# Optimization experiments

Hardware: AMD Instinct MI355X
Metric: run time of the kernel (lower is better)

## Reference

```python
import jax, jax.numpy as jnp
import numpy as np

N0, N1, B = 260000, 10240, 1024
E0, E1 = 256000, 10240
IN_C, HID, OUT_C = 602, 256, 41


def setup_inputs() -> dict:
    key = jax.random.key(0)
    ks = jax.random.split(key, 12)
    x = jax.random.normal(ks[0], (N0, IN_C), dtype=jnp.float32)
    W_l0 = jax.random.normal(ks[1], (IN_C, HID), dtype=jnp.float32) / np.sqrt(IN_C)
    b_l0 = jnp.zeros((HID,), dtype=jnp.float32)
    W_r0 = jax.random.normal(ks[2], (IN_C, HID), dtype=jnp.float32) / np.sqrt(IN_C)
    W_l1 = jax.random.normal(ks[3], (HID, OUT_C), dtype=jnp.float32) / np.sqrt(HID)
    b_l1 = jnp.zeros((OUT_C,), dtype=jnp.float32)
    W_r1 = jax.random.normal(ks[4], (HID, OUT_C), dtype=jnp.float32) / np.sqrt(HID)
    src0 = jax.random.randint(ks[5], (E0,), 0, N0)
    dst0 = jnp.sort(jax.random.randint(ks[6], (E0,), 0, N1))
    src1 = jax.random.randint(ks[7], (E1,), 0, N1)
    dst1 = jnp.sort(jax.random.randint(ks[8], (E1,), 0, B))
    return {"x": x, "W_l0": W_l0, "b_l0": b_l0, "W_r0": W_r0,
            "W_l1": W_l1, "b_l1": b_l1, "W_r1": W_r1,
            "src0": src0, "dst0": dst0, "src1": src1, "dst1": dst1}


def _sage_conv(x_src, x_tgt, src, dst, num_tgt, W_l, b_l, W_r):
    # mean aggregation of neighbor messages (PyG SAGEConv, mean aggr)
    msg = x_src[src]                                             # [E, C]
    s = jax.ops.segment_sum(msg, dst, num_segments=num_tgt)     # [Nt, C]
    cnt = jax.ops.segment_sum(jnp.ones((src.shape[0], 1), x_src.dtype),
                              dst, num_segments=num_tgt)         # [Nt, 1]
    agg = s / jnp.maximum(cnt, 1.0)
    # out = lin_l(agg) + lin_r(x_target); lin_r has no bias in PyG
    return agg @ W_l + b_l + x_tgt @ W_r


def reference(x, W_l0, b_l0, W_r0, W_l1, b_l1, W_r1, src0, dst0, src1, dst1):
    # layer 0: N0 sources -> N1 targets (targets are first N1 rows of x)
    h = _sage_conv(x, x[:N1], src0, dst0, N1, W_l0, b_l0, W_r0)
    h = jax.nn.relu(h)  # dropout is identity in eval mode
    # layer 1: N1 sources -> B targets
    out = _sage_conv(h, h[:B], src1, dst1, B, W_l1, b_l1, W_r1)
    return jax.nn.log_softmax(out, axis=-1)
```

## Files before the change

kernel.cpp:

```cpp
#include <hip/hip_runtime.h>
#include <hip/hip_bf16.h>
#include <math.h>

constexpr int cN1  = 10240;
constexpr int cB   = 1024;
constexpr int cE0  = 256000;
constexpr int cE1  = 10240;
constexpr int cIN  = 602;
constexpr int cHID = 256;
constexpr int cOUT = 41;
constexpr int KC   = 1216;

typedef __attribute__((ext_vector_type(8))) short short8;
typedef __attribute__((ext_vector_type(4))) float f32x4;

__device__ __forceinline__ int lower_bound_dev(const int* __restrict__ a, int n, int v) {
    int l = 0, r = n;
    while (l < r) { int m = (l + r) >> 1; if (a[m] < v) l = m + 1; else r = m; }
    return l;
}

__global__ __launch_bounds__(256) void k_agg0(
    const float* __restrict__ x, const int* __restrict__ src0,
    const int* __restrict__ dst0, __hip_bfloat16* __restrict__ cat)
{
    const int t   = blockIdx.x;
    const int tid = threadIdx.x;
    const int lo  = lower_bound_dev(dst0, cE0, t);
    const int hi  = lower_bound_dev(dst0, cE0, t + 1);
    const int cnt = hi - lo;

    float a0 = 0.f, a1 = 0.f, a2 = 0.f;
    __shared__ int s_src[256];
    for (int base = lo; base < hi; base += 256) {
        const int n = min(256, hi - base);
        __syncthreads();
        if (tid < n) s_src[tid] = src0[base + tid];
        __syncthreads();
        for (int j = 0; j < n; ++j) {
            const float* row = x + (long)s_src[j] * cIN;
            a0 += row[tid];
            a1 += row[tid + 256];
            if (tid < cIN - 512) a2 += row[tid + 512];
        }
    }

    const float inv = 1.f / (float)(cnt > 1 ? cnt : 1);
    __hip_bfloat16* cr = cat + (long)t * KC;
    const float*    xr = x   + (long)t * cIN;

    cr[tid]             = __float2bfloat16(a0 * inv);
    cr[tid + 256]       = __float2bfloat16(a1 * inv);
    cr[608 + tid]       = __float2bfloat16(xr[tid]);
    cr[608 + 256 + tid] = __float2bfloat16(xr[tid + 256]);
    if (tid < 96) {
        const float va = (tid < 90) ? a2 * inv      : 0.f;
        const float vx = (tid < 90) ? xr[512 + tid] : 0.f;
        cr[512 + tid]       = __float2bfloat16(va);
        cr[608 + 512 + tid] = __float2bfloat16(vx);
    }
}

__global__ __launch_bounds__(256) void k_prep_w(
    const float* __restrict__ Wl, const float* __restrict__ Wr,
    __hip_bfloat16* __restrict__ Wt)
{
    const int idx = blockIdx.x * 256 + threadIdx.x;
    const int n = idx / KC, k = idx - n * KC;
    float v = 0.f;
    if (k < cIN)                        v = Wl[(long)k * cHID + n];
    else if (k >= 608 && k < 608 + cIN) v = Wr[(long)(k - 608) * cHID + n];
    Wt[idx] = __float2bfloat16(v);
}

__global__ __launch_bounds__(256) void k_gemm(
    const __hip_bfloat16* __restrict__ cat, const __hip_bfloat16* __restrict__ Wt,
    const float* __restrict__ bias, float* __restrict__ h)
{
    const int tid  = threadIdx.x;
    const int m0   = (blockIdx.x >> 2) * 64;
    const int n0   = (blockIdx.x & 3) * 64;
    const int w    = tid >> 6, lane = tid & 63;
    const int wm   = (w & 1) * 32, wn = (w >> 1) * 32;
    const int lrow = lane & 15, quad = lane >> 4;

    __shared__ __hip_bfloat16 As[64 * 32];
    __shared__ __hip_bfloat16 Bs[64 * 32];

    f32x4 acc[2][2] = {};

    const int srow = tid >> 2, schunk = tid & 3;
    const __hip_bfloat16* gA = cat + (long)(m0 + srow) * KC + schunk * 8;
    const __hip_bfloat16* gB = Wt  + (long)(n0 + srow) * KC + schunk * 8;
    __hip_bfloat16* lA = As + srow * 32 + schunk * 8;
    __hip_bfloat16* lB = Bs + srow * 32 + schunk * 8;

    for (int k0 = 0; k0 < KC; k0 += 32) {
        const short8 av = *(const short8*)(gA + k0);
        const short8 bv = *(const short8*)(gB + k0);
        __syncthreads();
        *(short8*)lA = av;
        *(short8*)lB = bv;
        __syncthreads();

        short8 af[2], bf[2];
        #pragma unroll
        for (int f = 0; f < 2; ++f) {
            af[f] = *(const short8*)(As + (wm + f * 16 + lrow) * 32 + quad * 8);
            bf[f] = *(const short8*)(Bs + (wn + f * 16 + lrow) * 32 + quad * 8);
        }
        #pragma unroll
        for (int fm = 0; fm < 2; ++fm)
            #pragma unroll
            for (int fn = 0; fn < 2; ++fn)
                acc[fm][fn] = __builtin_amdgcn_mfma_f32_16x16x32_bf16(
                    af[fm], bf[fn], acc[fm][fn], 0, 0, 0);
    }

    #pragma unroll
    for (int fm = 0; fm < 2; ++fm)
        #pragma unroll
        for (int fn = 0; fn < 2; ++fn) {
            const int col = n0 + wn + fn * 16 + lrow;
            const float b = bias[col];
            #pragma unroll
            for (int r = 0; r < 4; ++r) {
                const int row = m0 + wm + fm * 16 + quad * 4 + r;
                h[(long)row * cHID + col] = fmaxf(acc[fm][fn][r] + b, 0.f);
            }
        }
}

__global__ __launch_bounds__(256) void k_agg1(
    const float* __restrict__ h, const int* __restrict__ src1,
    const int* __restrict__ dst1, float* __restrict__ agg1)
{
    const int t   = blockIdx.x;
    const int tid = threadIdx.x;
    const int lo  = lower_bound_dev(dst1, cE1, t);
    const int hi  = lower_bound_dev(dst1, cE1, t + 1);
    const int cnt = hi - lo;

    float a = 0.f;
    __shared__ int s_src[256];
    for (int base = lo; base < hi; base += 256) {
        const int n = min(256, hi - base);
        __syncthreads();
        if (tid < n) s_src[tid] = src1[base + tid];
        __syncthreads();
        for (int j = 0; j < n; ++j) a += h[(long)s_src[j] * cHID + tid];
    }
    agg1[(long)t * cHID + tid] = a / (float)(cnt > 1 ? cnt : 1);
}

__global__ __launch_bounds__(64) void k_out(
    const float* __restrict__ h,  const float* __restrict__ agg1,
    const float* __restrict__ Wl, const float* __restrict__ bias,
    const float* __restrict__ Wr, float* __restrict__ out)
{
    const int row = blockIdx.x;
    const int tid = threadIdx.x;
    __shared__ float sA[cHID], sH[cHID];
    for (int i = tid; i < cHID; i += 64) {
        sA[i] = agg1[(long)row * cHID + i];
        sH[i] = h[(long)row * cHID + i];
    }
    __syncthreads();

    float v = 0.f;
    if (tid < cOUT) {
        v = bias[tid];
        for (int k = 0; k < cHID; ++k)
            v += sA[k] * Wl[k * cOUT + tid] + sH[k] * Wr[k * cOUT + tid];
    }
    float lg = (tid < cOUT) ? v : -INFINITY;
    float m = lg;
    #pragma unroll
    for (int off = 32; off > 0; off >>= 1) m = fmaxf(m, __shfl_down(m, off));
    m = __shfl(m, 0);
    float e = (tid < cOUT) ? expf(v - m) : 0.f;
    float s = e;
    #pragma unroll
    for (int off = 32; off > 0; off >>= 1) s += __shfl_down(s, off);
    s = __shfl(s, 0);
    if (tid < cOUT) out[(long)row * cOUT + tid] = v - m - logf(s);
}

extern "C" void kernel_launch(void* const* d_in, const int* in_sizes, int n_in,
                              void* d_out, int out_size, void* d_ws, size_t ws_size,
                              hipStream_t stream)
{
    const float* x    = (const float*)d_in[0];
    const float* Wl0  = (const float*)d_in[1];
    const float* bl0  = (const float*)d_in[2];
    const float* Wr0  = (const float*)d_in[3];
    const float* Wl1  = (const float*)d_in[4];
    const float* bl1  = (const float*)d_in[5];
    const float* Wr1  = (const float*)d_in[6];
    const int*   src0 = (const int*)d_in[7];
    const int*   dst0 = (const int*)d_in[8];
    const int*   src1 = (const int*)d_in[9];
    const int*   dst1 = (const int*)d_in[10];
    float* out = (float*)d_out;

    char* ws = (char*)d_ws;
    const size_t szCat = (size_t)cN1 * KC * sizeof(__hip_bfloat16);
    const size_t szWt  = (size_t)cHID * KC * sizeof(__hip_bfloat16);
    const size_t szH   = (size_t)cN1 * cHID * sizeof(float);
    __hip_bfloat16* cat  = (__hip_bfloat16*)(ws);
    __hip_bfloat16* Wt   = (__hip_bfloat16*)(ws + szCat);
    float*          h    = (float*)(ws + szCat + szWt);
    float*          agg1 = (float*)(ws + szCat + szWt + szH);

    k_prep_w<<<(cHID * KC) / 256, 256, 0, stream>>>(Wl0, Wr0, Wt);
    k_agg0<<<cN1, 256, 0, stream>>>(x, src0, dst0, cat);
    k_gemm<<<(cN1 / 64) * 4, 256, 0, stream>>>(cat, Wt, bl0, h);
    k_agg1<<<cB, 256, 0, stream>>>(h, src1, dst1, agg1);
    k_out<<<cB, 64, 0, stream>>>(h, agg1, Wl1, bl1, Wr1, out);
}
```

Baseline: 867.5 us.

## Skip layer-0 aggregation for rows unused by layer 1, vectorize gather, swizzle GEMM

Two small kernels build a per-node flag. It marks the first B target rows and every node that appears as a layer-1 source. k_agg0 then returns early for unflagged rows, because their hidden features are never read downstream. The gather is also changed to float2 loads and bf16x2 stores, and the GEMM block index is remapped so that groups of M tiles share N tiles for better cache reuse. Unflagged rows of cat and h are left uninitialized and still pass through the GEMM, so the two extra launches add a little fixed overhead.

```diff
diff --git a/kernel.cpp b/kernel.cpp
--- a/kernel.cpp
+++ b/kernel.cpp
@@ -20,17 +20,32 @@
     return l;
 }
 
+__global__ __launch_bounds__(256) void k_flag_init(unsigned char* __restrict__ flag)
+{
+    const int i = blockIdx.x * 256 + threadIdx.x;
+    if (i < cN1) flag[i] = (i < cB) ? 1 : 0;
+}
+
+__global__ __launch_bounds__(256) void k_flag_mark(
+    const int* __restrict__ src1, unsigned char* __restrict__ flag)
+{
+    const int e = blockIdx.x * 256 + threadIdx.x;
+    if (e < cE1) flag[src1[e]] = 1;
+}
+
 __global__ __launch_bounds__(256) void k_agg0(
     const float* __restrict__ x, const int* __restrict__ src0,
-    const int* __restrict__ dst0, __hip_bfloat16* __restrict__ cat)
-{
-    const int t   = blockIdx.x;
+    const int* __restrict__ dst0, const unsigned char* __restrict__ flag,
+    __hip_bfloat16* __restrict__ cat)
+{
+    const int t = blockIdx.x;
+    if (!flag[t]) return;
     const int tid = threadIdx.x;
     const int lo  = lower_bound_dev(dst0, cE0, t);
     const int hi  = lower_bound_dev(dst0, cE0, t + 1);
     const int cnt = hi - lo;
 
-    float a0 = 0.f, a1 = 0.f, a2 = 0.f;
+    float ax = 0.f, ay = 0.f, bx = 0.f, by = 0.f;
     __shared__ int s_src[256];
     for (int base = lo; base < hi; base += 256) {
         const int n = min(256, hi - base);
@@ -38,26 +53,39 @@
         if (tid < n) s_src[tid] = src0[base + tid];
         __syncthreads();
         for (int j = 0; j < n; ++j) {
-            const float* row = x + (long)s_src[j] * cIN;
-            a0 += row[tid];
-            a1 += row[tid + 256];
-            if (tid < cIN - 512) a2 += row[tid + 512];
+            const float2* row2 = (const float2*)(x + (long)s_src[j] * cIN);
+            const float2 v = row2[tid];
+            ax += v.x; ay += v.y;
+            if (tid < 45) {
+                const float2 w = row2[256 + tid];
+                bx += w.x; by += w.y;
+            }
         }
     }
 
     const float inv = 1.f / (float)(cnt > 1 ? cnt : 1);
-    __hip_bfloat16* cr = cat + (long)t * KC;
-    const float*    xr = x   + (long)t * cIN;
-
-    cr[tid]             = __float2bfloat16(a0 * inv);
-    cr[tid + 256]       = __float2bfloat16(a1 * inv);
-    cr[608 + tid]       = __float2bfloat16(xr[tid]);
-    cr[608 + 256 + tid] = __float2bfloat16(xr[tid + 256]);
-    if (tid < 96) {
-        const float va = (tid < 90) ? a2 * inv      : 0.f;
-        const float vx = (tid < 90) ? xr[512 + tid] : 0.f;
-        cr[512 + tid]       = __float2bfloat16(va);
-        cr[608 + 512 + tid] = __float2bfloat16(vx);
+    __hip_bfloat162* cr2 = (__hip_bfloat162*)(cat + (long)t * KC);
+    const float2*    xr2 = (const float2*)(x + (long)t * cIN);
+
+    __hip_bfloat162 m2;
+    m2.x = __float2bfloat16(ax * inv); m2.y = __float2bfloat16(ay * inv);
+    cr2[tid] = m2;
+    const float2 xv = xr2[tid];
+    __hip_bfloat162 c2;
+    c2.x = __float2bfloat16(xv.x); c2.y = __float2bfloat16(xv.y);
+    cr2[304 + tid] = c2;
+    if (tid < 48) {
+        float mx = 0.f, my = 0.f, cx = 0.f, cy = 0.f;
+        if (tid < 45) {
+            mx = bx * inv; my = by * inv;
+            const float2 xw = xr2[256 + tid];
+            cx = xw.x; cy = xw.y;
+        }
+        __hip_bfloat162 ta, tb;
+        ta.x = __float2bfloat16(mx); ta.y = __float2bfloat16(my);
+        tb.x = __float2bfloat16(cx); tb.y = __float2bfloat16(cy);
+        cr2[256 + tid] = ta;
+        cr2[560 + tid] = tb;
     }
 }
 
@@ -77,9 +105,10 @@
     const __hip_bfloat16* __restrict__ cat, const __hip_bfloat16* __restrict__ Wt,
     const float* __restrict__ bias, float* __restrict__ h)
 {
+    const int bid  = blockIdx.x;
+    const int m0   = ((bid & 7) | ((bid >> 5) << 3)) * 64;
+    const int n0   = ((bid >> 3) & 3) * 64;
     const int tid  = threadIdx.x;
-    const int m0   = (blockIdx.x >> 2) * 64;
-    const int n0   = (blockIdx.x & 3) * 64;
     const int w    = tid >> 6, lane = tid & 63;
     const int wm   = (w & 1) * 32, wn = (w >> 1) * 32;
     const int lrow = lane & 15, quad = lane >> 4;
@@ -207,13 +236,17 @@
     const size_t szCat = (size_t)cN1 * KC * sizeof(__hip_bfloat16);
     const size_t szWt  = (size_t)cHID * KC * sizeof(__hip_bfloat16);
     const size_t szH   = (size_t)cN1 * cHID * sizeof(float);
+    const size_t szA1  = (size_t)cB * cHID * sizeof(float);
     __hip_bfloat16* cat  = (__hip_bfloat16*)(ws);
     __hip_bfloat16* Wt   = (__hip_bfloat16*)(ws + szCat);
     float*          h    = (float*)(ws + szCat + szWt);
     float*          agg1 = (float*)(ws + szCat + szWt + szH);
-
+    unsigned char*  flag = (unsigned char*)(ws + szCat + szWt + szH + szA1);
+
+    k_flag_init<<<cN1 / 256, 256, 0, stream>>>(flag);
+    k_flag_mark<<<cE1 / 256, 256, 0, stream>>>(src1, flag);
     k_prep_w<<<(cHID * KC) / 256, 256, 0, stream>>>(Wl0, Wr0, Wt);
-    k_agg0<<<cN1, 256, 0, stream>>>(x, src0, dst0, cat);
+    k_agg0<<<cN1, 256, 0, stream>>>(x, src0, dst0, flag, cat);
     k_gemm<<<(cN1 / 64) * 4, 256, 0, stream>>>(cat, Wt, bl0, h);
     k_agg1<<<cB, 256, 0, stream>>>(h, src1, dst1, agg1);
     k_out<<<cB, 64, 0, stream>>>(h, agg1, Wl1, bl1, Wr1, out);
```

New measurement: 836.0 us. -3.6%, faster.
